# Kernel optimization log

Hardware: AMD Instinct MI355X
Metric: run time of the kernel (lower is better)

## Reference

```python
import jax, jax.numpy as jnp
import numpy as np

B, N, F_IN = 2, 768, 10
FEATS = [F_IN, 128, 128, 64]  # DeepSet layer widths
D2 = 2 * FEATS[-1]            # lin2: cat of two broadcasts
H_MLP = 64                    # suffix hidden width
OUT = 1
SCALE = 0.05


def setup_inputs() -> dict:
    key = jax.random.key(0)
    ks = jax.random.split(key, 32)
    d = {"x": jax.random.normal(ks[0], (B, N, F_IN), dtype=jnp.float32)}
    i = 1
    for l, (ci, co) in enumerate(zip(FEATS[:-1], FEATS[1:])):
        d[f"w1_{l}"] = SCALE * jax.random.normal(ks[i], (co, ci), dtype=jnp.float32); i += 1
        d[f"b1_{l}"] = SCALE * jax.random.normal(ks[i], (co,), dtype=jnp.float32); i += 1
        d[f"w2_{l}"] = SCALE * jax.random.normal(ks[i], (co, ci), dtype=jnp.float32); i += 1
        d[f"b2_{l}"] = SCALE * jax.random.normal(ks[i], (co,), dtype=jnp.float32); i += 1
    d["sw0"] = SCALE * jax.random.normal(ks[i], (H_MLP, D2), dtype=jnp.float32); i += 1
    d["sb0"] = SCALE * jax.random.normal(ks[i], (H_MLP,), dtype=jnp.float32); i += 1
    d["sw1"] = SCALE * jax.random.normal(ks[i], (OUT, H_MLP), dtype=jnp.float32); i += 1
    d["sb1"] = SCALE * jax.random.normal(ks[i], (OUT,), dtype=jnp.float32)
    return d


def _deepset_layer(h, w1, b1, w2, b2):
    # h: (B, C, N). layer1(h) + layer2(h - mean_N(h)), both 1x1 convs.
    hm = h - h.mean(axis=2, keepdims=True)
    y = jnp.einsum('oc,bcn->bon', w1, h) + b1[None, :, None]
    y = y + jnp.einsum('oc,bcn->bon', w2, hm) + b2[None, :, None]
    return y


def reference(x, w1_0, b1_0, w2_0, b2_0, w1_1, b1_1, w2_1, b2_1,
              w1_2, b1_2, w2_2, b2_2, sw0, sb0, sw1, sb1):
    h = x.transpose(0, 2, 1)  # (B, F_IN, N)
    h = jax.nn.relu(_deepset_layer(h, w1_0, b1_0, w2_0, b2_0))
    h = jax.nn.relu(_deepset_layer(h, w1_1, b1_1, w2_1, b2_1))
    u = _deepset_layer(h, w1_2, b1_2, w2_2, b2_2)  # (B, f, N), no ReLU after last
    f = u.shape[1]
    # lin2 block: cat(m1, m2) over channels with m1[b,c,i,j]=u[b,c,j],
    # m2[b,c,i,j]=u[b,c,i]. The first 1x1 conv distributes over the concat:
    #   sw0 @ block = sw0[:, :f] @ m1 + sw0[:, f:] @ m2
    p = jnp.einsum('oc,bcn->bon', sw0[:, :f], u)   # contribution broadcast over i
    q = jnp.einsum('oc,bcn->bon', sw0[:, f:], u)   # contribution broadcast over j
    h1 = jax.nn.relu(p[:, :, None, :] + q[:, :, :, None] + sb0[None, :, None, None])  # (B, H, N, N)
    out = jnp.einsum('oc,bcij->boij', sw1, h1) + sb1[None, :, None, None]  # (B, 1, N, N)
    return out
```

## Files before the change

### kernel.cpp

```cpp
#include <hip/hip_runtime.h>

#define BB 2
#define NN 768
#define FIN 10

#define OFF0_OFF 0
#define S1_OFF   256
#define S2_OFF   512
#define H1_OFF   1024
#define H2_OFF   (H1_OFF + BB*128*NN)
#define U_OFF    (H2_OFF + BB*128*NN)
#define PP_OFF   (U_OFF + BB*64*NN)
#define QQ_OFF   (PP_OFF + BB*64*NN)

__global__ void k_meanx_off0(const float* __restrict__ x, const float* __restrict__ w2,
                             const float* __restrict__ b1, const float* __restrict__ b2,
                             float* __restrict__ off0)
{
    const int b = blockIdx.x, tid = threadIdx.x;
    __shared__ float red[FIN][256];
    __shared__ float mu[FIN];
    float acc[FIN];
#pragma unroll
    for (int c = 0; c < FIN; ++c) acc[c] = 0.f;
    for (int n = tid; n < NN; n += 256) {
        const float* xp = x + (b * NN + n) * FIN;
#pragma unroll
        for (int c = 0; c < FIN; ++c) acc[c] += xp[c];
    }
#pragma unroll
    for (int c = 0; c < FIN; ++c) red[c][tid] = acc[c];
    __syncthreads();
    for (int s = 128; s > 0; s >>= 1) {
        if (tid < s) {
#pragma unroll
            for (int c = 0; c < FIN; ++c) red[c][tid] += red[c][tid + s];
        }
        __syncthreads();
    }
    if (tid < FIN) mu[tid] = red[tid][0] * (1.f / (float)NN);
    __syncthreads();
    if (tid < 128) {
        float o = b1[tid] + b2[tid];
#pragma unroll
        for (int c = 0; c < FIN; ++c) o -= w2[tid * FIN + c] * mu[c];
        off0[b * 128 + tid] = o;
    }
}

__global__ void k_layer0(const float* __restrict__ x, const float* __restrict__ w1,
                         const float* __restrict__ w2, const float* __restrict__ off0,
                         float* __restrict__ h1, float* __restrict__ s1)
{
    const int b = blockIdx.x, n0 = blockIdx.y * 128, o0 = blockIdx.z * 32, tid = threadIdx.x;
    __shared__ alignas(16) float xt[FIN][128];
    __shared__ alignas(16) float wl[FIN][36];
    __shared__ float offs[32];
    __shared__ float red[8][4][33];
    for (int idx = tid; idx < FIN * 128; idx += 256) {
        int nn = idx / FIN, c = idx % FIN;
        xt[c][nn] = x[(b * NN + n0 + nn) * FIN + c];
    }
    for (int idx = tid; idx < 32 * FIN; idx += 256) {
        int o = idx / FIN, c = idx % FIN;
        wl[c][o] = w1[(o0 + o) * FIN + c] + w2[(o0 + o) * FIN + c];
    }
    if (tid < 32) offs[tid] = off0[b * 128 + o0 + tid];
    __syncthreads();
    const int tx = tid & 31, ty = tid >> 5;
    float4 acc[4];
#pragma unroll
    for (int a = 0; a < 4; ++a) {
        float o = offs[ty * 4 + a];
        acc[a] = make_float4(o, o, o, o);
    }
#pragma unroll
    for (int c = 0; c < FIN; ++c) {
        float4 xv = *reinterpret_cast<const float4*>(&xt[c][tx * 4]);
        float4 wv = *reinterpret_cast<const float4*>(&wl[c][ty * 4]);
        float wa[4] = {wv.x, wv.y, wv.z, wv.w};
#pragma unroll
        for (int a = 0; a < 4; ++a) {
            acc[a].x += wa[a] * xv.x;
            acc[a].y += wa[a] * xv.y;
            acc[a].z += wa[a] * xv.z;
            acc[a].w += wa[a] * xv.w;
        }
    }
#pragma unroll
    for (int a = 0; a < 4; ++a) {
        float4 r;
        r.x = fmaxf(acc[a].x, 0.f);
        r.y = fmaxf(acc[a].y, 0.f);
        r.z = fmaxf(acc[a].z, 0.f);
        r.w = fmaxf(acc[a].w, 0.f);
        *reinterpret_cast<float4*>(&h1[((size_t)(b * 128 + o0 + ty * 4 + a)) * NN + n0 + tx * 4]) = r;
        red[ty][a][tx] = r.x + r.y + r.z + r.w;
    }
    __syncthreads();
    if (tid < 32) {
        float s = 0.f;
#pragma unroll
        for (int t = 0; t < 32; ++t) s += red[tid >> 2][tid & 3][t];
        atomicAdd(&s1[b * 128 + o0 + tid], s);
    }
}

template <int COUT, bool RELU, bool COLSUM>
__global__ void k_layer(const float* __restrict__ hin, const float* __restrict__ w1,
                        const float* __restrict__ b1, const float* __restrict__ b2,
                        const float* __restrict__ w2, const float* __restrict__ csum,
                        float* __restrict__ hout, float* __restrict__ sout)
{
    const int b = blockIdx.x, n0 = blockIdx.y * 64, o0 = blockIdx.z * 32, tid = threadIdx.x;
    __shared__ alignas(16) float hl[128][64];
    __shared__ float wl[128][37];
    __shared__ float mul[128];
    __shared__ float offp[32][9];
    __shared__ float red[16][2][17];
    for (int idx = tid; idx < 128 * 64; idx += 256) {
        int c = idx >> 6, nn = idx & 63;
        hl[c][nn] = hin[((size_t)(b * 128 + c)) * NN + n0 + nn];
    }
    for (int idx = tid; idx < 128 * 32; idx += 256) {
        int o = idx >> 7, c = idx & 127;
        wl[c][o] = w1[(o0 + o) * 128 + c] + w2[(o0 + o) * 128 + c];
    }
    if (tid < 128) mul[tid] = csum[b * 128 + tid] * (1.f / (float)NN);
    __syncthreads();
    {
        int o = tid >> 3, part = tid & 7;
        float p = 0.f;
        const float* w2r = w2 + (o0 + o) * 128 + part * 16;
        const float* mr = mul + part * 16;
#pragma unroll
        for (int i = 0; i < 16; ++i) p += w2r[i] * mr[i];
        offp[o][part] = p;
    }
    const int tx = tid & 15, ty = tid >> 4;
    float4 acc0 = {0, 0, 0, 0}, acc1 = {0, 0, 0, 0};
#pragma unroll 8
    for (int c = 0; c < 128; ++c) {
        float4 hv = *reinterpret_cast<const float4*>(&hl[c][tx * 4]);
        float w0 = wl[c][ty * 2], w1v = wl[c][ty * 2 + 1];
        acc0.x += w0 * hv.x;
        acc0.y += w0 * hv.y;
        acc0.z += w0 * hv.z;
        acc0.w += w0 * hv.w;
        acc1.x += w1v * hv.x;
        acc1.y += w1v * hv.y;
        acc1.z += w1v * hv.z;
        acc1.w += w1v * hv.w;
    }
    __syncthreads();
#pragma unroll
    for (int a = 0; a < 2; ++a) {
        int o = ty * 2 + a;
        float off = b1[o0 + o] + b2[o0 + o];
#pragma unroll
        for (int p = 0; p < 8; ++p) off -= offp[o][p];
        float4 r = a ? acc1 : acc0;
        r.x += off; r.y += off; r.z += off; r.w += off;
        if (RELU) {
            r.x = fmaxf(r.x, 0.f);
            r.y = fmaxf(r.y, 0.f);
            r.z = fmaxf(r.z, 0.f);
            r.w = fmaxf(r.w, 0.f);
        }
        *reinterpret_cast<float4*>(&hout[((size_t)(b * COUT + o0 + o)) * NN + n0 + tx * 4]) = r;
        if (COLSUM) red[ty][a][tx] = r.x + r.y + r.z + r.w;
    }
    if (COLSUM) {
        __syncthreads();
        if (tid < 32) {
            float s = 0.f;
#pragma unroll
            for (int t = 0; t < 16; ++t) s += red[tid >> 1][tid & 1][t];
            atomicAdd(&sout[b * 128 + o0 + tid], s);
        }
    }
}

__global__ void k_pq(const float* __restrict__ u, const float* __restrict__ sw0,
                     const float* __restrict__ sb0, float* __restrict__ pp,
                     float* __restrict__ qq)
{
    const int b = blockIdx.x, n0 = blockIdx.y * 64, ch0 = blockIdx.z * 32, tid = threadIdx.x;
    __shared__ alignas(16) float ul[64][64];
    __shared__ float wl[64][37];
    __shared__ float bs[32];
    for (int idx = tid; idx < 64 * 64; idx += 256) {
        int c = idx >> 6, nn = idx & 63;
        ul[c][nn] = u[((size_t)(b * 64 + c)) * NN + n0 + nn];
    }
    for (int idx = tid; idx < 64 * 32; idx += 256) {
        int o = idx >> 6, c = idx & 63;
        int ch = ch0 + o;
        wl[c][o] = (ch < 64) ? sw0[ch * 128 + c] : sw0[(ch - 64) * 128 + 64 + c];
    }
    if (tid < 32) {
        int ch = ch0 + tid;
        bs[tid] = (ch < 64) ? sb0[ch] : 0.f;
    }
    __syncthreads();
    const int tx = tid & 15, ty = tid >> 4;
    float b0 = bs[ty * 2], b1v = bs[ty * 2 + 1];
    float4 acc0 = {b0, b0, b0, b0}, acc1 = {b1v, b1v, b1v, b1v};
#pragma unroll 8
    for (int c = 0; c < 64; ++c) {
        float4 hv = *reinterpret_cast<const float4*>(&ul[c][tx * 4]);
        float w0 = wl[c][ty * 2], w1v = wl[c][ty * 2 + 1];
        acc0.x += w0 * hv.x;
        acc0.y += w0 * hv.y;
        acc0.z += w0 * hv.z;
        acc0.w += w0 * hv.w;
        acc1.x += w1v * hv.x;
        acc1.y += w1v * hv.y;
        acc1.z += w1v * hv.z;
        acc1.w += w1v * hv.w;
    }
#pragma unroll
    for (int a = 0; a < 2; ++a) {
        int ch = ch0 + ty * 2 + a;
        float4 r = a ? acc1 : acc0;
        float* dst = (ch < 64) ? (pp + ((size_t)(b * 64 + ch)) * NN)
                               : (qq + ((size_t)(b * 64 + ch - 64)) * NN);
        *reinterpret_cast<float4*>(&dst[n0 + tx * 4]) = r;
    }
}

__global__ void k_final(const float* __restrict__ pp, const float* __restrict__ qq,
                        const float* __restrict__ sw1, const float* __restrict__ sb1,
                        float* __restrict__ out)
{
    const int b = blockIdx.x, i0 = blockIdx.y * 64, j0 = blockIdx.z * 64, tid = threadIdx.x;
    __shared__ alignas(16) float pl[64][64];
    __shared__ alignas(16) float ql[64][64];
    __shared__ float wl[64];
    __shared__ float sbv;
    for (int idx = tid; idx < 4096; idx += 512) {
        int c = idx >> 6, k = idx & 63;
        pl[c][k] = pp[((size_t)(b * 64 + c)) * NN + j0 + k];
        ql[c][k] = qq[((size_t)(b * 64 + c)) * NN + i0 + k];
    }
    if (tid < 64) wl[tid] = sw1[tid];
    if (tid == 0) sbv = sb1[0];
    __syncthreads();
    const int tx = tid & 15, ty = tid >> 4;
    float sb = sbv;
    float4 acc0 = {sb, sb, sb, sb}, acc1 = {sb, sb, sb, sb};
#pragma unroll 8
    for (int c = 0; c < 64; ++c) {
        float4 pv = *reinterpret_cast<const float4*>(&pl[c][tx * 4]);
        float q0 = ql[c][ty * 2], q1 = ql[c][ty * 2 + 1];
        float w = wl[c];
        acc0.x += w * fmaxf(pv.x + q0, 0.f);
        acc0.y += w * fmaxf(pv.y + q0, 0.f);
        acc0.z += w * fmaxf(pv.z + q0, 0.f);
        acc0.w += w * fmaxf(pv.w + q0, 0.f);
        acc1.x += w * fmaxf(pv.x + q1, 0.f);
        acc1.y += w * fmaxf(pv.y + q1, 0.f);
        acc1.z += w * fmaxf(pv.z + q1, 0.f);
        acc1.w += w * fmaxf(pv.w + q1, 0.f);
    }
    size_t base = (size_t)b * NN * NN + (size_t)(i0 + ty * 2) * NN + j0 + tx * 4;
    *reinterpret_cast<float4*>(&out[base]) = acc0;
    *reinterpret_cast<float4*>(&out[base + NN]) = acc1;
}

extern "C" void kernel_launch(void* const* d_in, const int* in_sizes, int n_in,
                              void* d_out, int out_size, void* d_ws, size_t ws_size,
                              hipStream_t stream)
{
    const float* x    = (const float*)d_in[0];
    const float* w1_0 = (const float*)d_in[1];
    const float* b1_0 = (const float*)d_in[2];
    const float* w2_0 = (const float*)d_in[3];
    const float* b2_0 = (const float*)d_in[4];
    const float* w1_1 = (const float*)d_in[5];
    const float* b1_1 = (const float*)d_in[6];
    const float* w2_1 = (const float*)d_in[7];
    const float* b2_1 = (const float*)d_in[8];
    const float* w1_2 = (const float*)d_in[9];
    const float* b1_2 = (const float*)d_in[10];
    const float* w2_2 = (const float*)d_in[11];
    const float* b2_2 = (const float*)d_in[12];
    const float* sw0  = (const float*)d_in[13];
    const float* sb0  = (const float*)d_in[14];
    const float* sw1  = (const float*)d_in[15];
    const float* sb1  = (const float*)d_in[16];

    float* ws   = (float*)d_ws;
    float* off0 = ws + OFF0_OFF;
    float* s1   = ws + S1_OFF;
    float* s2   = ws + S2_OFF;
    float* h1   = ws + H1_OFF;
    float* h2   = ws + H2_OFF;
    float* u    = ws + U_OFF;
    float* pp   = ws + PP_OFF;
    float* qq   = ws + QQ_OFF;

    (void)hipMemsetAsync(ws + S1_OFF, 0, 512 * sizeof(float), stream);

    k_meanx_off0<<<BB, 256, 0, stream>>>(x, w2_0, b1_0, b2_0, off0);
    k_layer0<<<dim3(BB, 6, 4), 256, 0, stream>>>(x, w1_0, w2_0, off0, h1, s1);
    k_layer<128, true, true><<<dim3(BB, 12, 4), 256, 0, stream>>>(h1, w1_1, b1_1, b2_1, w2_1, s1, h2, s2);
    k_layer<64, false, false><<<dim3(BB, 12, 2), 256, 0, stream>>>(h2, w1_2, b1_2, b2_2, w2_2, s2, u, nullptr);
    k_pq<<<dim3(BB, 12, 4), 256, 0, stream>>>(u, sw0, sb0, pp, qq);
    k_final<<<dim3(BB, 12, 12), 512, 0, stream>>>(pp, qq, sw1, sb1, (float*)d_out);
}
```

Baseline: 51.58 us.

## Fold last DeepSet layer into pq projection and drop atomics/memset

Precomputes the product of sw0 with the combined last-layer weights so that p and q come straight from h2, which removes the separate u layer kernel and its round trip through memory. Column sums are now written as per-block partials and summed by the consumer, replacing the memset and atomics. The mean-of-x kernel is merged into layer0, which now computes all 128 output channels per block. Fewer launches and less intermediate traffic, paid for with fewer blocks in layer0, a bigger tile per block in layer1, and a small extra weight-product kernel on every call.

```diff
diff --git a/kernel.cpp b/kernel.cpp
--- a/kernel.cpp
+++ b/kernel.cpp
@@ -4,22 +4,57 @@
 #define NN 768
 #define FIN 10
 
-#define OFF0_OFF 0
-#define S1_OFF   256
-#define S2_OFF   512
-#define H1_OFF   1024
-#define H2_OFF   (H1_OFF + BB*128*NN)
-#define U_OFF    (H2_OFF + BB*128*NN)
-#define PP_OFF   (U_OFF + BB*64*NN)
-#define QQ_OFF   (PP_OFF + BB*64*NN)
-
-__global__ void k_meanx_off0(const float* __restrict__ x, const float* __restrict__ w2,
-                             const float* __restrict__ b1, const float* __restrict__ b2,
-                             float* __restrict__ off0)
-{
-    const int b = blockIdx.x, tid = threadIdx.x;
-    __shared__ float red[FIN][256];
+#define WPQ_OFF 0
+#define S1P_OFF 16384
+#define S2P_OFF (S1P_OFF + BB*6*128)
+#define H1_OFF  (S2P_OFF + BB*12*128)
+#define H2_OFF  (H1_OFF + BB*128*NN)
+#define PP_OFF  (H2_OFF + BB*128*NN)
+#define QQ_OFF  (PP_OFF + BB*64*NN)
+
+__global__ void k_wpq(const float* __restrict__ sw0, const float* __restrict__ w1_2,
+                      const float* __restrict__ w2_2, float* __restrict__ wpq)
+{
+    const int o0 = blockIdx.x * 16, tid = threadIdx.x;
+    __shared__ float w2l[64][132];
+    __shared__ float sl[16][64];
+    for (int idx = tid; idx < 2048; idx += 256) {
+        int k = idx >> 5, c4 = (idx & 31) * 4;
+        float4 a = *(const float4*)&w1_2[k * 128 + c4];
+        float4 b = *(const float4*)&w2_2[k * 128 + c4];
+        float4 r = {a.x + b.x, a.y + b.y, a.z + b.z, a.w + b.w};
+        *(float4*)&w2l[k][c4] = r;
+    }
+    for (int idx = tid; idx < 16 * 64; idx += 256) {
+        int o = idx >> 6, k = idx & 63;
+        int oo = o0 + o;
+        sl[o][k] = (oo < 64) ? sw0[oo * 128 + k] : sw0[(oo - 64) * 128 + 64 + k];
+    }
+    __syncthreads();
+    const int tx = tid & 31, ty = tid >> 5;
+    float4 a0 = {0, 0, 0, 0}, a1 = {0, 0, 0, 0};
+    for (int k = 0; k < 64; ++k) {
+        float4 wv = *(const float4*)&w2l[k][tx * 4];
+        float s0 = sl[ty * 2][k], s1 = sl[ty * 2 + 1][k];
+        a0.x += s0 * wv.x; a0.y += s0 * wv.y; a0.z += s0 * wv.z; a0.w += s0 * wv.w;
+        a1.x += s1 * wv.x; a1.y += s1 * wv.y; a1.z += s1 * wv.z; a1.w += s1 * wv.w;
+    }
+    *(float4*)&wpq[(o0 + ty * 2) * 128 + tx * 4] = a0;
+    *(float4*)&wpq[(o0 + ty * 2 + 1) * 128 + tx * 4] = a1;
+}
+
+__global__ void k_layer0(const float* __restrict__ x, const float* __restrict__ w1,
+                         const float* __restrict__ w2, const float* __restrict__ b1,
+                         const float* __restrict__ b2, float* __restrict__ h1,
+                         float* __restrict__ s1p)
+{
+    const int b = blockIdx.x, nblk = blockIdx.y, n0 = nblk * 128, tid = threadIdx.x;
+    __shared__ float red[FIN][257];
     __shared__ float mu[FIN];
+    __shared__ float xt[FIN][128];
+    __shared__ float wl[FIN][128];
+    __shared__ float offs[128];
+    __shared__ float red2[8][16][33];
     float acc[FIN];
 #pragma unroll
     for (int c = 0; c < FIN; ++c) acc[c] = 0.f;
@@ -39,193 +74,211 @@
         __syncthreads();
     }
     if (tid < FIN) mu[tid] = red[tid][0] * (1.f / (float)NN);
+    for (int idx = tid; idx < FIN * 128; idx += 256) {
+        int n = idx / FIN, c = idx % FIN;
+        xt[c][n] = x[(b * NN + n0 + n) * FIN + c];
+    }
+    for (int idx = tid; idx < FIN * 128; idx += 256) {
+        int o = idx / FIN, c = idx % FIN;
+        wl[c][o] = w1[o * FIN + c] + w2[o * FIN + c];
+    }
     __syncthreads();
     if (tid < 128) {
         float o = b1[tid] + b2[tid];
 #pragma unroll
         for (int c = 0; c < FIN; ++c) o -= w2[tid * FIN + c] * mu[c];
-        off0[b * 128 + tid] = o;
-    }
-}
-
-__global__ void k_layer0(const float* __restrict__ x, const float* __restrict__ w1,
-                         const float* __restrict__ w2, const float* __restrict__ off0,
-                         float* __restrict__ h1, float* __restrict__ s1)
-{
-    const int b = blockIdx.x, n0 = blockIdx.y * 128, o0 = blockIdx.z * 32, tid = threadIdx.x;
-    __shared__ alignas(16) float xt[FIN][128];
-    __shared__ alignas(16) float wl[FIN][36];
-    __shared__ float offs[32];
-    __shared__ float red[8][4][33];
-    for (int idx = tid; idx < FIN * 128; idx += 256) {
-        int nn = idx / FIN, c = idx % FIN;
-        xt[c][nn] = x[(b * NN + n0 + nn) * FIN + c];
-    }
-    for (int idx = tid; idx < 32 * FIN; idx += 256) {
-        int o = idx / FIN, c = idx % FIN;
-        wl[c][o] = w1[(o0 + o) * FIN + c] + w2[(o0 + o) * FIN + c];
-    }
-    if (tid < 32) offs[tid] = off0[b * 128 + o0 + tid];
+        offs[tid] = o;
+    }
     __syncthreads();
     const int tx = tid & 31, ty = tid >> 5;
+    float4 av[16];
+#pragma unroll
+    for (int a = 0; a < 16; ++a) {
+        float o = offs[ty * 16 + a];
+        av[a] = make_float4(o, o, o, o);
+    }
+#pragma unroll
+    for (int c = 0; c < FIN; ++c) {
+        float4 xv = *(const float4*)&xt[c][tx * 4];
+#pragma unroll
+        for (int a = 0; a < 16; ++a) {
+            float w = wl[c][ty * 16 + a];
+            av[a].x += w * xv.x; av[a].y += w * xv.y;
+            av[a].z += w * xv.z; av[a].w += w * xv.w;
+        }
+    }
+#pragma unroll
+    for (int a = 0; a < 16; ++a) {
+        float4 r = av[a];
+        r.x = fmaxf(r.x, 0.f); r.y = fmaxf(r.y, 0.f);
+        r.z = fmaxf(r.z, 0.f); r.w = fmaxf(r.w, 0.f);
+        *(float4*)&h1[((size_t)(b * 128 + ty * 16 + a)) * NN + n0 + tx * 4] = r;
+        red2[ty][a][tx] = r.x + r.y + r.z + r.w;
+    }
+    __syncthreads();
+    if (tid < 128) {
+        float s = 0.f;
+#pragma unroll
+        for (int t = 0; t < 32; ++t) s += red2[tid >> 4][tid & 15][t];
+        s1p[(b * 6 + nblk) * 128 + tid] = s;
+    }
+}
+
+__global__ void k_layer1(const float* __restrict__ h1, const float* __restrict__ w1,
+                         const float* __restrict__ b1, const float* __restrict__ w2,
+                         const float* __restrict__ b2, const float* __restrict__ s1p,
+                         float* __restrict__ h2, float* __restrict__ s2p)
+{
+    const int b = blockIdx.x, nblk = blockIdx.y, n0 = nblk * 64,
+              o0 = blockIdx.z * 64, tid = threadIdx.x;
+    __shared__ float hl[128][64];
+    __shared__ float wl[64][132];
+    __shared__ float mul[128];
+    __shared__ float offp[4][64];
+    __shared__ float offs[64];
+    __shared__ float red[16][4][17];
+    if (tid < 128) {
+        float s = 0.f;
+#pragma unroll
+        for (int k = 0; k < 6; ++k) s += s1p[(b * 6 + k) * 128 + tid];
+        mul[tid] = s * (1.f / (float)NN);
+    }
+    for (int idx = tid; idx < 2048; idx += 256) {
+        int c = idx >> 4, n4 = (idx & 15) * 4;
+        *(float4*)&hl[c][n4] = *(const float4*)&h1[((size_t)(b * 128 + c)) * NN + n0 + n4];
+    }
+    for (int idx = tid; idx < 2048; idx += 256) {
+        int o = idx >> 5, c4 = (idx & 31) * 4;
+        float4 a = *(const float4*)&w1[(o0 + o) * 128 + c4];
+        float4 bb = *(const float4*)&w2[(o0 + o) * 128 + c4];
+        float4 r = {a.x + bb.x, a.y + bb.y, a.z + bb.z, a.w + bb.w};
+        *(float4*)&wl[o][c4] = r;
+    }
+    __syncthreads();
+    {
+        int o = tid & 63, part = tid >> 6;
+        const float* w2r = w2 + (o0 + o) * 128 + part * 32;
+        const float* mr = mul + part * 32;
+        float p = 0.f;
+#pragma unroll
+        for (int i = 0; i < 32; ++i) p += w2r[i] * mr[i];
+        offp[part][o] = p;
+    }
+    __syncthreads();
+    if (tid < 64)
+        offs[tid] = b1[o0 + tid] + b2[o0 + tid]
+                  - offp[0][tid] - offp[1][tid] - offp[2][tid] - offp[3][tid];
+    __syncthreads();
+    const int tx = tid & 15, ty = tid >> 4;
     float4 acc[4];
 #pragma unroll
+    for (int a = 0; a < 4; ++a) acc[a] = make_float4(0.f, 0.f, 0.f, 0.f);
+    for (int c = 0; c < 128; ++c) {
+        float4 hv = *(const float4*)&hl[c][tx * 4];
+#pragma unroll
+        for (int a = 0; a < 4; ++a) {
+            float w = wl[ty * 4 + a][c];
+            acc[a].x += w * hv.x; acc[a].y += w * hv.y;
+            acc[a].z += w * hv.z; acc[a].w += w * hv.w;
+        }
+    }
+#pragma unroll
     for (int a = 0; a < 4; ++a) {
-        float o = offs[ty * 4 + a];
-        acc[a] = make_float4(o, o, o, o);
-    }
-#pragma unroll
-    for (int c = 0; c < FIN; ++c) {
-        float4 xv = *reinterpret_cast<const float4*>(&xt[c][tx * 4]);
-        float4 wv = *reinterpret_cast<const float4*>(&wl[c][ty * 4]);
-        float wa[4] = {wv.x, wv.y, wv.z, wv.w};
+        int o = ty * 4 + a;
+        float off = offs[o];
+        float4 r = acc[a];
+        r.x = fmaxf(r.x + off, 0.f); r.y = fmaxf(r.y + off, 0.f);
+        r.z = fmaxf(r.z + off, 0.f); r.w = fmaxf(r.w + off, 0.f);
+        *(float4*)&h2[((size_t)(b * 128 + o0 + o)) * NN + n0 + tx * 4] = r;
+        red[ty][a][tx] = r.x + r.y + r.z + r.w;
+    }
+    __syncthreads();
+    if (tid < 64) {
+        float s = 0.f;
+#pragma unroll
+        for (int t = 0; t < 16; ++t) s += red[tid >> 2][tid & 3][t];
+        s2p[(b * 12 + nblk) * 128 + o0 + tid] = s;
+    }
+}
+
+__global__ void k_pq(const float* __restrict__ h2, const float* __restrict__ wpq,
+                     const float* __restrict__ b1_2, const float* __restrict__ w2_2,
+                     const float* __restrict__ b2_2, const float* __restrict__ sw0,
+                     const float* __restrict__ sb0, const float* __restrict__ s2p,
+                     float* __restrict__ pp, float* __restrict__ qq)
+{
+    const int b = blockIdx.x, nblk = blockIdx.y, n0 = nblk * 64,
+              z = blockIdx.z, o0 = z * 64, tid = threadIdx.x;
+    __shared__ float hl[128][64];
+    __shared__ float wl[64][132];
+    __shared__ float mul[128];
+    __shared__ float offp[4][64];
+    __shared__ float off2[64];
+    __shared__ float bp[4][64];
+    __shared__ float bias[64];
+    if (tid < 128) {
+        float s = 0.f;
+#pragma unroll
+        for (int k = 0; k < 12; ++k) s += s2p[(b * 12 + k) * 128 + tid];
+        mul[tid] = s * (1.f / (float)NN);
+    }
+    for (int idx = tid; idx < 2048; idx += 256) {
+        int c = idx >> 4, n4 = (idx & 15) * 4;
+        *(float4*)&hl[c][n4] = *(const float4*)&h2[((size_t)(b * 128 + c)) * NN + n0 + n4];
+    }
+    for (int idx = tid; idx < 2048; idx += 256) {
+        int o = idx >> 5, c4 = (idx & 31) * 4;
+        *(float4*)&wl[o][c4] = *(const float4*)&wpq[(o0 + o) * 128 + c4];
+    }
+    __syncthreads();
+    {
+        int k = tid & 63, part = tid >> 6;
+        const float* w2r = w2_2 + k * 128 + part * 32;
+        const float* mr = mul + part * 32;
+        float p = 0.f;
+#pragma unroll
+        for (int i = 0; i < 32; ++i) p += w2r[i] * mr[i];
+        offp[part][k] = p;
+    }
+    __syncthreads();
+    if (tid < 64)
+        off2[tid] = b1_2[tid] + b2_2[tid]
+                  - offp[0][tid] - offp[1][tid] - offp[2][tid] - offp[3][tid];
+    __syncthreads();
+    {
+        int o = tid & 63, part = tid >> 6;
+        const float* srow = sw0 + o * 128 + (z ? 64 : 0) + part * 16;
+        float p = 0.f;
+#pragma unroll
+        for (int i = 0; i < 16; ++i) p += srow[i] * off2[part * 16 + i];
+        bp[part][o] = p;
+    }
+    __syncthreads();
+    if (tid < 64)
+        bias[tid] = bp[0][tid] + bp[1][tid] + bp[2][tid] + bp[3][tid]
+                  + (z == 0 ? sb0[tid] : 0.f);
+    __syncthreads();
+    const int tx = tid & 15, ty = tid >> 4;
+    float4 acc[4];
+#pragma unroll
+    for (int a = 0; a < 4; ++a) acc[a] = make_float4(0.f, 0.f, 0.f, 0.f);
+    for (int c = 0; c < 128; ++c) {
+        float4 hv = *(const float4*)&hl[c][tx * 4];
 #pragma unroll
         for (int a = 0; a < 4; ++a) {
-            acc[a].x += wa[a] * xv.x;
-            acc[a].y += wa[a] * xv.y;
-            acc[a].z += wa[a] * xv.z;
-            acc[a].w += wa[a] * xv.w;
+            float w = wl[ty * 4 + a][c];
+            acc[a].x += w * hv.x; acc[a].y += w * hv.y;
+            acc[a].z += w * hv.z; acc[a].w += w * hv.w;
         }
     }
+    float* dst = (z == 0) ? pp : qq;
 #pragma unroll
     for (int a = 0; a < 4; ++a) {
-        float4 r;
-        r.x = fmaxf(acc[a].x, 0.f);
-        r.y = fmaxf(acc[a].y, 0.f);
-        r.z = fmaxf(acc[a].z, 0.f);
-        r.w = fmaxf(acc[a].w, 0.f);
-        *reinterpret_cast<float4*>(&h1[((size_t)(b * 128 + o0 + ty * 4 + a)) * NN + n0 + tx * 4]) = r;
-        red[ty][a][tx] = r.x + r.y + r.z + r.w;
-    }
-    __syncthreads();
-    if (tid < 32) {
-        float s = 0.f;
-#pragma unroll
-        for (int t = 0; t < 32; ++t) s += red[tid >> 2][tid & 3][t];
-        atomicAdd(&s1[b * 128 + o0 + tid], s);
-    }
-}
-
-template <int COUT, bool RELU, bool COLSUM>
-__global__ void k_layer(const float* __restrict__ hin, const float* __restrict__ w1,
-                        const float* __restrict__ b1, const float* __restrict__ b2,
-                        const float* __restrict__ w2, const float* __restrict__ csum,
-                        float* __restrict__ hout, float* __restrict__ sout)
-{
-    const int b = blockIdx.x, n0 = blockIdx.y * 64, o0 = blockIdx.z * 32, tid = threadIdx.x;
-    __shared__ alignas(16) float hl[128][64];
-    __shared__ float wl[128][37];
-    __shared__ float mul[128];
-    __shared__ float offp[32][9];
-    __shared__ float red[16][2][17];
-    for (int idx = tid; idx < 128 * 64; idx += 256) {
-        int c = idx >> 6, nn = idx & 63;
-        hl[c][nn] = hin[((size_t)(b * 128 + c)) * NN + n0 + nn];
-    }
-    for (int idx = tid; idx < 128 * 32; idx += 256) {
-        int o = idx >> 7, c = idx & 127;
-        wl[c][o] = w1[(o0 + o) * 128 + c] + w2[(o0 + o) * 128 + c];
-    }
-    if (tid < 128) mul[tid] = csum[b * 128 + tid] * (1.f / (float)NN);
-    __syncthreads();
-    {
-        int o = tid >> 3, part = tid & 7;
-        float p = 0.f;
-        const float* w2r = w2 + (o0 + o) * 128 + part * 16;
-        const float* mr = mul + part * 16;
-#pragma unroll
-        for (int i = 0; i < 16; ++i) p += w2r[i] * mr[i];
-        offp[o][part] = p;
-    }
-    const int tx = tid & 15, ty = tid >> 4;
-    float4 acc0 = {0, 0, 0, 0}, acc1 = {0, 0, 0, 0};
-#pragma unroll 8
-    for (int c = 0; c < 128; ++c) {
-        float4 hv = *reinterpret_cast<const float4*>(&hl[c][tx * 4]);
-        float w0 = wl[c][ty * 2], w1v = wl[c][ty * 2 + 1];
-        acc0.x += w0 * hv.x;
-        acc0.y += w0 * hv.y;
-        acc0.z += w0 * hv.z;
-        acc0.w += w0 * hv.w;
-        acc1.x += w1v * hv.x;
-        acc1.y += w1v * hv.y;
-        acc1.z += w1v * hv.z;
-        acc1.w += w1v * hv.w;
-    }
-    __syncthreads();
-#pragma unroll
-    for (int a = 0; a < 2; ++a) {
-        int o = ty * 2 + a;
-        float off = b1[o0 + o] + b2[o0 + o];
-#pragma unroll
-        for (int p = 0; p < 8; ++p) off -= offp[o][p];
-        float4 r = a ? acc1 : acc0;
-        r.x += off; r.y += off; r.z += off; r.w += off;
-        if (RELU) {
-            r.x = fmaxf(r.x, 0.f);
-            r.y = fmaxf(r.y, 0.f);
-            r.z = fmaxf(r.z, 0.f);
-            r.w = fmaxf(r.w, 0.f);
-        }
-        *reinterpret_cast<float4*>(&hout[((size_t)(b * COUT + o0 + o)) * NN + n0 + tx * 4]) = r;
-        if (COLSUM) red[ty][a][tx] = r.x + r.y + r.z + r.w;
-    }
-    if (COLSUM) {
-        __syncthreads();
-        if (tid < 32) {
-            float s = 0.f;
-#pragma unroll
-            for (int t = 0; t < 16; ++t) s += red[tid >> 1][tid & 1][t];
-            atomicAdd(&sout[b * 128 + o0 + tid], s);
-        }
-    }
-}
-
-__global__ void k_pq(const float* __restrict__ u, const float* __restrict__ sw0,
-                     const float* __restrict__ sb0, float* __restrict__ pp,
-                     float* __restrict__ qq)
-{
-    const int b = blockIdx.x, n0 = blockIdx.y * 64, ch0 = blockIdx.z * 32, tid = threadIdx.x;
-    __shared__ alignas(16) float ul[64][64];
-    __shared__ float wl[64][37];
-    __shared__ float bs[32];
-    for (int idx = tid; idx < 64 * 64; idx += 256) {
-        int c = idx >> 6, nn = idx & 63;
-        ul[c][nn] = u[((size_t)(b * 64 + c)) * NN + n0 + nn];
-    }
-    for (int idx = tid; idx < 64 * 32; idx += 256) {
-        int o = idx >> 6, c = idx & 63;
-        int ch = ch0 + o;
-        wl[c][o] = (ch < 64) ? sw0[ch * 128 + c] : sw0[(ch - 64) * 128 + 64 + c];
-    }
-    if (tid < 32) {
-        int ch = ch0 + tid;
-        bs[tid] = (ch < 64) ? sb0[ch] : 0.f;
-    }
-    __syncthreads();
-    const int tx = tid & 15, ty = tid >> 4;
-    float b0 = bs[ty * 2], b1v = bs[ty * 2 + 1];
-    float4 acc0 = {b0, b0, b0, b0}, acc1 = {b1v, b1v, b1v, b1v};
-#pragma unroll 8
-    for (int c = 0; c < 64; ++c) {
-        float4 hv = *reinterpret_cast<const float4*>(&ul[c][tx * 4]);
-        float w0 = wl[c][ty * 2], w1v = wl[c][ty * 2 + 1];
-        acc0.x += w0 * hv.x;
-        acc0.y += w0 * hv.y;
-        acc0.z += w0 * hv.z;
-        acc0.w += w0 * hv.w;
-        acc1.x += w1v * hv.x;
-        acc1.y += w1v * hv.y;
-        acc1.z += w1v * hv.z;
-        acc1.w += w1v * hv.w;
-    }
-#pragma unroll
-    for (int a = 0; a < 2; ++a) {
-        int ch = ch0 + ty * 2 + a;
-        float4 r = a ? acc1 : acc0;
-        float* dst = (ch < 64) ? (pp + ((size_t)(b * 64 + ch)) * NN)
-                               : (qq + ((size_t)(b * 64 + ch - 64)) * NN);
-        *reinterpret_cast<float4*>(&dst[n0 + tx * 4]) = r;
+        int o = ty * 4 + a;
+        float bb = bias[o];
+        float4 r = acc[a];
+        r.x += bb; r.y += bb; r.z += bb; r.w += bb;
+        *(float4*)&dst[((size_t)(b * 64 + o)) * NN + n0 + tx * 4] = r;
     }
 }
 
@@ -234,8 +287,8 @@
                         float* __restrict__ out)
 {
     const int b = blockIdx.x, i0 = blockIdx.y * 64, j0 = blockIdx.z * 64, tid = threadIdx.x;
-    __shared__ alignas(16) float pl[64][64];
-    __shared__ alignas(16) float ql[64][64];
+    __shared__ float pl[64][64];
+    __shared__ float ql[64][64];
     __shared__ float wl[64];
     __shared__ float sbv;
     for (int idx = tid; idx < 4096; idx += 512) {
@@ -251,7 +304,7 @@
     float4 acc0 = {sb, sb, sb, sb}, acc1 = {sb, sb, sb, sb};
 #pragma unroll 8
     for (int c = 0; c < 64; ++c) {
-        float4 pv = *reinterpret_cast<const float4*>(&pl[c][tx * 4]);
+        float4 pv = *(const float4*)&pl[c][tx * 4];
         float q0 = ql[c][ty * 2], q1 = ql[c][ty * 2 + 1];
         float w = wl[c];
         acc0.x += w * fmaxf(pv.x + q0, 0.f);
@@ -264,8 +317,8 @@
         acc1.w += w * fmaxf(pv.w + q1, 0.f);
     }
     size_t base = (size_t)b * NN * NN + (size_t)(i0 + ty * 2) * NN + j0 + tx * 4;
-    *reinterpret_cast<float4*>(&out[base]) = acc0;
-    *reinterpret_cast<float4*>(&out[base + NN]) = acc1;
+    *(float4*)&out[base] = acc0;
+    *(float4*)&out[base + NN] = acc1;
 }
 
 extern "C" void kernel_launch(void* const* d_in, const int* in_sizes, int n_in,
@@ -291,21 +344,17 @@
     const float* sb1  = (const float*)d_in[16];
 
     float* ws   = (float*)d_ws;
-    float* off0 = ws + OFF0_OFF;
-    float* s1   = ws + S1_OFF;
-    float* s2   = ws + S2_OFF;
+    float* wpq  = ws + WPQ_OFF;
+    float* s1p  = ws + S1P_OFF;
+    float* s2p  = ws + S2P_OFF;
     float* h1   = ws + H1_OFF;
     float* h2   = ws + H2_OFF;
-    float* u    = ws + U_OFF;
     float* pp   = ws + PP_OFF;
     float* qq   = ws + QQ_OFF;
 
-    (void)hipMemsetAsync(ws + S1_OFF, 0, 512 * sizeof(float), stream);
-
-    k_meanx_off0<<<BB, 256, 0, stream>>>(x, w2_0, b1_0, b2_0, off0);
-    k_layer0<<<dim3(BB, 6, 4), 256, 0, stream>>>(x, w1_0, w2_0, off0, h1, s1);
-    k_layer<128, true, true><<<dim3(BB, 12, 4), 256, 0, stream>>>(h1, w1_1, b1_1, b2_1, w2_1, s1, h2, s2);
-    k_layer<64, false, false><<<dim3(BB, 12, 2), 256, 0, stream>>>(h2, w1_2, b1_2, b2_2, w2_2, s2, u, nullptr);
-    k_pq<<<dim3(BB, 12, 4), 256, 0, stream>>>(u, sw0, sb0, pp, qq);
-    k_final<<<dim3(BB, 12, 12), 512, 0, stream>>>(pp, qq, sw1, sb1, (float*)d_out);
-}
+    k_wpq   <<<8, 256, 0, stream>>>(sw0, w1_2, w2_2, wpq);
+    k_layer0<<<dim3(BB, 6), 256, 0, stream>>>(x, w1_0, w2_0, b1_0, b2_0, h1, s1p);
+    k_layer1<<<dim3(BB, 12, 2), 256, 0, stream>>>(h1, w1_1, b1_1, w2_1, b2_1, s1p, h2, s2p);
+    k_pq    <<<dim3(BB, 12, 2), 256, 0, stream>>>(h2, wpq, b1_2, w2_2, b2_2, sw0, sb0, s2p, pp, qq);
+    k_final <<<dim3(BB, 12, 12), 512, 0, stream>>>(pp, qq, sw1, sb1, (float*)d_out);
+}
```

Result: slower. 52.85 us (+2.4%).
